# Kernel optimization log

Measured on AMD Instinct MI355X. Metric: run time of the kernel, lower is better.

## Reference

```python
import jax, jax.numpy as jnp
import numpy as np

NUM_HEADS = 16
NEG_INF = -9e15


def setup_inputs() -> dict:
    key = jax.random.key(0)
    k1, k2, k3 = jax.random.split(key, 3)
    B, S, D = 2, 2048, 1024
    # xavier-uniform-ish init scale for weights
    lim_qkv = float(np.sqrt(6.0 / (D + 3 * D)))
    lim_o = float(np.sqrt(6.0 / (D + D)))
    return {
        "x": jax.random.normal(k1, (B, S, D), dtype=jnp.float32),
        "w_qkv": jax.random.uniform(k2, (3 * D, D), minval=-lim_qkv, maxval=lim_qkv, dtype=jnp.float32),
        "b_qkv": jnp.zeros((3 * D,), dtype=jnp.float32),
        "w_o": jax.random.uniform(k3, (D, D), minval=-lim_o, maxval=lim_o, dtype=jnp.float32),
        "b_o": jnp.zeros((D,), dtype=jnp.float32),
    }


def reference(x, w_qkv, b_qkv, w_o, b_o):
    B, S, D = x.shape
    H = NUM_HEADS
    hd = D // H
    # qkv projection: [B,S,3D]
    qkv = x @ w_qkv.T + b_qkv
    # -> [B, H, S, 3*hd], then split
    qkv = qkv.reshape(B, S, H, 3 * hd).transpose(0, 2, 1, 3)
    q, k, v = jnp.split(qkv, 3, axis=-1)  # each [B,H,S,hd]
    scale = 1.0 / jnp.sqrt(jnp.asarray(hd, dtype=x.dtype))
    logits = jnp.einsum("bhqd,bhkd->bhqk", q, k) * scale
    attn = jax.nn.softmax(logits, axis=-1)
    vals = jnp.einsum("bhqk,bhkd->bhqd", attn, v)
    vals = vals.transpose(0, 2, 1, 3).reshape(B, S, D)
    return vals @ w_o.T + b_o
```

## Files before the change

kernel.cpp:

```cpp
#include <hip/hip_runtime.h>
#include <math.h>

#define NHEADS 16
#define HD 64

typedef __attribute__((ext_vector_type(8))) _Float16 half8;
typedef __attribute__((ext_vector_type(4))) _Float16 half4;
typedef __attribute__((ext_vector_type(4))) float f32x4;
typedef __attribute__((ext_vector_type(16))) float f32x16;
typedef __attribute__((ext_vector_type(4))) unsigned int u32x4;

__device__ inline void load_lds16(const void* g, void* l) {
    __builtin_amdgcn_global_load_lds(
        (const __attribute__((address_space(1))) unsigned int*)g,
        (__attribute__((address_space(3))) unsigned int*)l, 16, 0, 0);
}
__device__ inline void pl32swap(unsigned int& x, unsigned int& y) {
    asm volatile("v_permlane32_swap_b32 %0, %1" : "+v"(x), "+v"(y));
}

#define NX  4194304
#define NWQ 3145728
#define NWO 1048576
__global__ void cvt_all(const float* __restrict__ x, const float* __restrict__ wq,
                        const float* __restrict__ wo, _Float16* __restrict__ xf,
                        _Float16* __restrict__ wqf, _Float16* __restrict__ wof) {
    int i = (blockIdx.x * blockDim.x + threadIdx.x) * 8;
    const float* src; _Float16* dst; int off;
    if (i < NX)            { src = x;  dst = xf;  off = i; }
    else if (i < NX + NWQ) { src = wq; dst = wqf; off = i - NX; }
    else                   { src = wo; dst = wof; off = i - (NX + NWQ); }
    float4 a = *(const float4*)(src + off);
    float4 b = *(const float4*)(src + off + 4);
    half8 h;
    h[0] = (_Float16)a.x; h[1] = (_Float16)a.y; h[2] = (_Float16)a.z; h[3] = (_Float16)a.w;
    h[4] = (_Float16)b.x; h[5] = (_Float16)b.y; h[6] = (_Float16)b.z; h[7] = (_Float16)b.w;
    *(half8*)(dst + off) = h;
}

#define GEMM_SETUP(K, NTILE)                                                           \
    const int tid = threadIdx.x;                                                       \
    const int l = tid & 63, w = tid >> 6;                                              \
    const int wr = w >> 1, wc = w & 1;                                                 \
    const int nwg = gridDim.x * gridDim.y;                                             \
    const int bid = blockIdx.y * gridDim.x + blockIdx.x;                               \
    const int swz = (bid & 7) * (nwg >> 3) + (bid >> 3);                               \
    const int m0 = (swz / gridDim.x) * 128, n0 = (swz % gridDim.x) * (NTILE);          \
    const int srow = tid >> 2;                                                         \
    const int schunk = (tid & 3) ^ ((srow >> 1) & 3);                                  \
    const size_t gA0 = (size_t)(m0 + srow) * K + schunk * 8;                           \
    const size_t gA1 = gA0 + (size_t)64 * K;                                           \
    const size_t gB0 = (size_t)(n0 + srow) * K + schunk * 8;                           \
    unsigned char* ldsW = smem + w * 1024;                                             \
    const int col16 = l & 15, kc = l >> 4;                                             \
    const int ra0 = wr * 64 + col16;                                                   \
    const int offA = ra0 * 64 + ((kc ^ ((ra0 >> 1) & 3)) * 16);

#define QSCALE 0.18033688f
__global__ __launch_bounds__(256, 2) void gemm_qkv(
    const _Float16* __restrict__ A, const _Float16* __restrict__ B,
    const float* __restrict__ bias,
    _Float16* __restrict__ Qf, _Float16* __restrict__ Kf,
    _Float16* __restrict__ VfT, int K) {
    __shared__ __align__(1024) unsigned char smem[49152];
    GEMM_SETUP(K, 128)
    const size_t gB1 = gB0 + (size_t)64 * K;
    const int rb0 = wc * 64 + col16;
    const int offB = rb0 * 64 + ((kc ^ ((rb0 >> 1) & 3)) * 16);
    f32x4 acc[4][4] = {};

#define GSTAGE(k0_, buf_)                                                              \
    load_lds16(A + gA0 + (k0_), ldsW + (buf_) * 16384 + 0);                            \
    load_lds16(A + gA1 + (k0_), ldsW + (buf_) * 16384 + 4096);                         \
    load_lds16(B + gB0 + (k0_), ldsW + (buf_) * 16384 + 8192);                         \
    load_lds16(B + gB1 + (k0_), ldsW + (buf_) * 16384 + 12288);
#define GSTEP(s_, buf_, VM, dostage)                                                   \
    asm volatile("s_waitcnt " VM ::: "memory");                                        \
    __builtin_amdgcn_sched_barrier(0);                                                 \
    __builtin_amdgcn_s_barrier();                                                      \
    if (dostage) { GSTAGE(((s_) + 2) * 32, ((buf_) + 2) % 3) }                         \
    {                                                                                  \
        const unsigned char* bs = smem + (buf_) * 16384;                               \
        half8 af[4], bf[4];                                                            \
        _Pragma("unroll")                                                              \
        for (int m = 0; m < 4; ++m) af[m] = *(const half8*)(bs + offA + m * 1024);     \
        _Pragma("unroll")                                                              \
        for (int n = 0; n < 4; ++n) bf[n] = *(const half8*)(bs + 8192 + offB + n * 1024); \
        _Pragma("unroll")                                                              \
        for (int m = 0; m < 4; ++m)                                                    \
            _Pragma("unroll")                                                          \
            for (int n = 0; n < 4; ++n)                                                \
                acc[m][n] = __builtin_amdgcn_mfma_f32_16x16x32_f16(af[m], bf[n], acc[m][n], 0, 0, 0); \
    }

    GSTAGE(0, 0)
    GSTAGE(32, 1)
    for (int t = 0; t < 30; t += 3) {
        GSTEP(t, 0, "vmcnt(4)", 1)
        GSTEP(t + 1, 1, "vmcnt(4)", 1)
        GSTEP(t + 2, 2, "vmcnt(4)", 1)
    }
    GSTEP(30, 0, "vmcnt(4)", 0)
    GSTEP(31, 1, "vmcnt(0)", 0)
#undef GSTAGE
#undef GSTEP

    const int rowb = m0 + wr * 64 + (l >> 4) * 4;
    const int colb = n0 + wc * 64 + col16;
    #pragma unroll
    for (int n = 0; n < 4; ++n) {
        int col = colb + n * 16;
        int h = col / 192;
        int rem = col - h * 192;
        int part = rem >> 6, d = rem & 63;
        float bv = bias[col];
        #pragma unroll
        for (int m = 0; m < 4; ++m) {
            int r0 = rowb + m * 16;
            int b = r0 >> 11, s0r = r0 & 2047;
            int bh = b * 16 + h;
            if (part == 0) {
                #pragma unroll
                for (int j = 0; j < 4; ++j)
                    Qf[((size_t)bh * 2048 + s0r + j) * 64 + d] =
                        (_Float16)((acc[m][n][j] + bv) * QSCALE);
            } else if (part == 1) {
                #pragma unroll
                for (int j = 0; j < 4; ++j)
                    Kf[((size_t)bh * 2048 + s0r + j) * 64 + d] = (_Float16)(acc[m][n][j] + bv);
            } else {
                half4 pk;
                pk[0] = (_Float16)(acc[m][n][0] + bv);
                pk[1] = (_Float16)(acc[m][n][1] + bv);
                pk[2] = (_Float16)(acc[m][n][2] + bv);
                pk[3] = (_Float16)(acc[m][n][3] + bv);
                *(half4*)&VfT[((size_t)bh * 64 + d) * 2048 + s0r] = pk;
            }
        }
    }
}

__global__ __launch_bounds__(256, 2) void gemm_o(
    const _Float16* __restrict__ A, const _Float16* __restrict__ B,
    const float* __restrict__ bias, float* __restrict__ C,
    int M, int N, int K) {
    __shared__ __align__(1024) unsigned char smem[36864];
    GEMM_SETUP(K, 64)
    const int rb0 = wc * 32 + col16;
    const int offB = rb0 * 64 + ((kc ^ ((rb0 >> 1) & 3)) * 16);
    f32x4 acc[4][2] = {};

#define OSTAGE(k0_, buf_)                                                              \
    load_lds16(A + gA0 + (k0_), ldsW + (buf_) * 12288 + 0);                            \
    load_lds16(A + gA1 + (k0_), ldsW + (buf_) * 12288 + 4096);                         \
    load_lds16(B + gB0 + (k0_), ldsW + (buf_) * 12288 + 8192);
#define OSTEP(s_, buf_, VM, dostage)                                                   \
    asm volatile("s_waitcnt " VM ::: "memory");                                        \
    __builtin_amdgcn_sched_barrier(0);                                                 \
    __builtin_amdgcn_s_barrier();                                                      \
    if (dostage) { OSTAGE(((s_) + 2) * 32, ((buf_) + 2) % 3) }                         \
    {                                                                                  \
        const unsigned char* bs = smem + (buf_) * 12288;                               \
        half8 af[4], bf[2];                                                            \
        _Pragma("unroll")                                                              \
        for (int m = 0; m < 4; ++m) af[m] = *(const half8*)(bs + offA + m * 1024);     \
        _Pragma("unroll")                                                              \
        for (int n = 0; n < 2; ++n) bf[n] = *(const half8*)(bs + 8192 + offB + n * 1024); \
        _Pragma("unroll")                                                              \
        for (int m = 0; m < 4; ++m)                                                    \
            _Pragma("unroll")                                                          \
            for (int n = 0; n < 2; ++n)                                                \
                acc[m][n] = __builtin_amdgcn_mfma_f32_16x16x32_f16(af[m], bf[n], acc[m][n], 0, 0, 0); \
    }

    OSTAGE(0, 0)
    OSTAGE(32, 1)
    for (int t = 0; t < 30; t += 3) {
        OSTEP(t, 0, "vmcnt(3)", 1)
        OSTEP(t + 1, 1, "vmcnt(3)", 1)
        OSTEP(t + 2, 2, "vmcnt(3)", 1)
    }
    OSTEP(30, 0, "vmcnt(3)", 0)
    OSTEP(31, 1, "vmcnt(0)", 0)
#undef OSTAGE
#undef OSTEP

    const int rowb = m0 + wr * 64 + (l >> 4) * 4;
    const int colb = n0 + wc * 32 + col16;
    float bv[2];
    #pragma unroll
    for (int n = 0; n < 2; ++n) bv[n] = bias[colb + n * 16];
    #pragma unroll
    for (int m = 0; m < 4; ++m)
        #pragma unroll
        for (int j = 0; j < 4; ++j) {
            float* crow = C + (size_t)(rowb + m * 16 + j) * N + colb;
            #pragma unroll
            for (int n = 0; n < 2; ++n) crow[n * 16] = acc[m][n][j] + bv[n];
        }
}

__global__ __launch_bounds__(512, 2) void mfma_attn(
    const _Float16* __restrict__ Qf, const _Float16* __restrict__ Kf,
    const _Float16* __restrict__ VfT, _Float16* __restrict__ vals) {
    __shared__ __align__(1024) unsigned char smem[49152];
    const int tid = threadIdx.x;
    const int l = tid & 63, w = tid >> 6;
    const int l31 = l & 31, hl = l >> 5;
    const int hwbid = blockIdx.y * gridDim.x + blockIdx.x;
    const int q_t = (hwbid >> 3) & 7;
    const int bh = (hwbid & 7) + ((hwbid >> 6) << 3);
    const int q0 = q_t * 256;
    const int h = bh & 15, b = bh >> 4;

    half8 qf[4];
    {
        const _Float16* qp = Qf + ((size_t)bh * 2048 + q0 + w * 32 + l31) * 64 + hl * 8;
        #pragma unroll
        for (int c = 0; c < 4; ++c) qf[c] = *(const half8*)(qp + c * 16);
    }
    f32x16 zvec = {};
    f32x16 o0 = {}, o1 = {};
    float mshift = 0.f, lsum = 0.f;

    const _Float16* Kg = Kf + (size_t)bh * 2048 * 64;
    const _Float16* Vg = VfT + (size_t)bh * 64 * 2048;

    int offK, offV;
    {
        int row2 = w * 4 + (l >> 4);
        int slot = (l & 15) ^ (row2 & 15);
        int row = row2 * 2 + (slot >> 3);
        int chunk = slot & 7;
        offK = row * 64 + chunk * 8;
        offV = row * 2048 + chunk * 8;
    }
    const int sbase = (l31 & 1) * 8;
    const int xr = (l31 >> 1) & 15;
    const int rb0 = (l31 >> 1) * 256;

    #define STAGE(kt0, buf)                                                            \
        {                                                                              \
            unsigned char* bK = smem + (buf) * 8192 + w * 1024;                        \
            unsigned char* bV = smem + 24576 + (buf) * 8192 + w * 1024;                \
            load_lds16(Kg + (size_t)(kt0) * 64 + offK, bK);                            \
            load_lds16(Vg + (kt0) + offV, bV);                                         \
        }

    #define QK_TILE(kb, D0, D1)                                                        \
        {                                                                              \
            const unsigned char* Ksb_ = smem + (kb) * 8192;                            \
            {                                                                          \
                int chOff = ((sbase + hl) ^ xr) << 4;                                  \
                half8 k0_ = *(const half8*)(Ksb_ + rb0 + chOff);                       \
                half8 k1_ = *(const half8*)(Ksb_ + rb0 + 4096 + chOff);                \
                D0 = __builtin_amdgcn_mfma_f32_32x32x16_f16(k0_, qf[0], zvec, 0, 0, 0);\
                D1 = __builtin_amdgcn_mfma_f32_32x32x16_f16(k1_, qf[0], zvec, 0, 0, 0);\
            }                                                                          \
            _Pragma("unroll")                                                          \
            for (int kc = 1; kc < 4; ++kc) {                                           \
                int chOff = ((sbase + kc * 2 + hl) ^ xr) << 4;                         \
                half8 k0_ = *(const half8*)(Ksb_ + rb0 + chOff);                       \
                half8 k1_ = *(const half8*)(Ksb_ + rb0 + 4096 + chOff);                \
                D0 = __builtin_amdgcn_mfma_f32_32x32x16_f16(k0_, qf[kc], D0, 0, 0, 0); \
                D1 = __builtin_amdgcn_mfma_f32_32x32x16_f16(k1_, qf[kc], D1, 0, 0, 0); \
            }                                                                          \
        }

    #define SMPV(S0, S1, vb_)                                                          \
        {                                                                              \
            const unsigned char* Vsb_ = smem + 24576 + (vb_) * 8192;                   \
            if (__any(mshift != 0.f)) {                                                \
                _Pragma("unroll")                                                      \
                for (int r = 0; r < 16; ++r) { S0[r] -= mshift; S1[r] -= mshift; }     \
            }                                                                          \
            float r0 = 0.f, r1 = 0.f, r2 = 0.f, r3 = 0.f;                              \
            unsigned int a[2][8];                                                      \
            _Pragma("unroll")                                                          \
            for (int j = 0; j < 8; ++j) {                                              \
                float p0 = __builtin_amdgcn_exp2f(S0[2 * j]);                          \
                float p1 = __builtin_amdgcn_exp2f(S0[2 * j + 1]);                      \
                float q0_ = __builtin_amdgcn_exp2f(S1[2 * j]);                         \
                float q1_ = __builtin_amdgcn_exp2f(S1[2 * j + 1]);                     \
                r0 += p0; r1 += p1; r2 += q0_; r3 += q1_;                              \
                a[0][j] = __builtin_bit_cast(unsigned int, __builtin_amdgcn_cvt_pkrtz(p0, p1));   \
                a[1][j] = __builtin_bit_cast(unsigned int, __builtin_amdgcn_cvt_pkrtz(q0_, q1_)); \
            }                                                                          \
            float rsum = (r0 + r1) + (r2 + r3);                                        \
            if (__any(rsum > 32768.f)) {                                               \
                float pmax = S0[0];                                                    \
                _Pragma("unroll")                                                      \
                for (int r = 1; r < 16; ++r) pmax = fmaxf(pmax, S0[r]);                \
                _Pragma("unroll")                                                      \
                for (int r = 0; r < 16; ++r) pmax = fmaxf(pmax, S1[r]);                \
                pmax = fmaxf(pmax, __shfl_xor(pmax, 32, 64));                          \
                float d_ = fmaxf(pmax, 0.f);                                           \
                float corr = __builtin_amdgcn_exp2f(-d_);                              \
                _Pragma("unroll")                                                      \
                for (int r = 0; r < 16; ++r) { S0[r] -= d_; S1[r] -= d_; }             \
                _Pragma("unroll")                                                      \
                for (int r = 0; r < 16; ++r) { o0[r] *= corr; o1[r] *= corr; }         \
                lsum *= corr;                                                          \
                mshift += d_;                                                          \
                r0 = r1 = r2 = r3 = 0.f;                                               \
                _Pragma("unroll")                                                      \
                for (int j = 0; j < 8; ++j) {                                          \
                    float p0 = __builtin_amdgcn_exp2f(S0[2 * j]);                      \
                    float p1 = __builtin_amdgcn_exp2f(S0[2 * j + 1]);                  \
                    float q0_ = __builtin_amdgcn_exp2f(S1[2 * j]);                     \
                    float q1_ = __builtin_amdgcn_exp2f(S1[2 * j + 1]);                 \
                    r0 += p0; r1 += p1; r2 += q0_; r3 += q1_;                          \
                    a[0][j] = __builtin_bit_cast(unsigned int, __builtin_amdgcn_cvt_pkrtz(p0, p1));   \
                    a[1][j] = __builtin_bit_cast(unsigned int, __builtin_amdgcn_cvt_pkrtz(q0_, q1_)); \
                }                                                                      \
                rsum = (r0 + r1) + (r2 + r3);                                          \
            }                                                                          \
            lsum += rsum;                                                              \
            _Pragma("unroll")                                                          \
            for (int c = 0; c < 2; ++c) {                                              \
                pl32swap(a[c][0], a[c][2]);                                            \
                pl32swap(a[c][1], a[c][3]);                                            \
                pl32swap(a[c][4], a[c][6]);                                            \
                pl32swap(a[c][5], a[c][7]);                                            \
            }                                                                          \
            _Pragma("unroll")                                                          \
            for (int kk = 0; kk < 4; ++kk) {                                           \
                u32x4 pw;                                                              \
                pw.x = a[kk >> 1][(kk & 1) * 4 + 0];                                   \
                pw.y = a[kk >> 1][(kk & 1) * 4 + 1];                                   \
                pw.z = a[kk >> 1][(kk & 1) * 4 + 2];                                   \
                pw.w = a[kk >> 1][(kk & 1) * 4 + 3];                                   \
                half8 pf = __builtin_bit_cast(half8, pw);                              \
                int chOff = ((sbase + kk * 2 + hl) ^ xr) << 4;                         \
                half8 v0 = *(const half8*)(Vsb_ + rb0 + chOff);                        \
                half8 v1 = *(const half8*)(Vsb_ + rb0 + 4096 + chOff);                 \
                o0 = __builtin_amdgcn_mfma_f32_32x32x16_f16(v0, pf, o0, 0, 0, 0);      \
                o1 = __builtin_amdgcn_mfma_f32_32x32x16_f16(v1, pf, o1, 0, 0, 0);      \
            }                                                                          \
        }

    #define AITER(tt, kb, VM, dostage)                                                 \
        asm volatile("s_waitcnt " VM ::: "memory");                                    \
        __builtin_amdgcn_sched_barrier(0);                                             \
        __builtin_amdgcn_s_barrier();                                                  \
        if (dostage) STAGE(((tt) + 2) * 64, ((kb) + 2) % 3)                            \
        QK_TILE(kb, sS0, sS1)                                                          \
        SMPV(sS0, sS1, kb)

    STAGE(0, 0)
    STAGE(64, 1)
    f32x16 sS0, sS1;
    for (int t = 0; t < 30; t += 3) {
        AITER(t, 0, "vmcnt(2)", 1)
        AITER(t + 1, 1, "vmcnt(2)", 1)
        AITER(t + 2, 2, "vmcnt(2)", 1)
    }
    AITER(30, 0, "vmcnt(2)", 0)
    AITER(31, 1, "vmcnt(0)", 0)

    lsum += __shfl_xor(lsum, 32, 64);
    float inv = 1.f / lsum;
    size_t orow = ((size_t)(b * 2048 + q0 + w * 32 + l31)) * 1024 + h * 64;
    #pragma unroll
    for (int dc = 0; dc < 2; ++dc) {
        const f32x16* op = dc ? &o1 : &o0;
        #pragma unroll
        for (int rq = 0; rq < 4; ++rq) {
            int d0 = dc * 32 + rq * 8 + hl * 4;
            half4 hv;
            #pragma unroll
            for (int j = 0; j < 4; ++j) hv[j] = (_Float16)((*op)[rq * 4 + j] * inv);
            *(half4*)(vals + orow + d0) = hv;
        }
    }
}

extern "C" void kernel_launch(void* const* d_in, const int* in_sizes, int n_in,
                              void* d_out, int out_size, void* d_ws, size_t ws_size,
                              hipStream_t stream) {
    const float* x     = (const float*)d_in[0];
    const float* w_qkv = (const float*)d_in[1];
    const float* b_qkv = (const float*)d_in[2];
    const float* w_o   = (const float*)d_in[3];
    const float* b_o   = (const float*)d_in[4];
    float* out = (float*)d_out;

    const int B = 2, S = 2048, D = 1024;
    const int M = B * S;
    const int N1 = 3 * D;
    const int BH = B * NHEADS;

    _Float16* xf  = (_Float16*)d_ws;
    _Float16* wqf = xf  + (size_t)M * D;
    _Float16* wof = wqf + (size_t)N1 * D;
    _Float16* Qf  = wof + (size_t)D * D;
    _Float16* Kf  = Qf  + (size_t)BH * S * HD;
    _Float16* VfT = Kf  + (size_t)BH * S * HD;
    _Float16* vals = xf;

    cvt_all<<<(NX + NWQ + NWO) / 2048, 256, 0, stream>>>(x, w_qkv, w_o, xf, wqf, wof);

    gemm_qkv<<<dim3(N1 / 128, M / 128), 256, 0, stream>>>(xf, wqf, b_qkv, Qf, Kf, VfT, D);

    mfma_attn<<<dim3(S / 256, BH), 512, 0, stream>>>(Qf, Kf, VfT, vals);

    gemm_o<<<dim3(D / 64, M / 128), 256, 0, stream>>>(vals, wof, b_o, out, M, D, D);
}
```

Measured before the change: 107.2 us.

## Rewrite QKV GEMM with 256x256 tiles, 8 waves and phased double-buffered loads

Replaces the 128x128 QKV projection GEMM (256 threads, triple-buffered K=32 stages) with a 256x256 tile per workgroup. It uses 8 waves and a double-buffered K=64 pipeline whose global-to-LDS loads are split into four compute phases, with s_setprio raised around the MFMA blocks. The larger tile is meant to raise arithmetic intensity and cut redundant global/LDS traffic per output. In exchange it uses 128KB of LDS, so only one block fits per CU, and the grid shrinks to 192 workgroups, which leaves some CUs idle. It also renames a loop variable in the attention kernel and inlines the old setup macro into gemm_o.

```diff
diff --git a/kernel.cpp b/kernel.cpp
--- a/kernel.cpp
+++ b/kernel.cpp
@@ -38,74 +38,107 @@
     *(half8*)(dst + off) = h;
 }
 
-#define GEMM_SETUP(K, NTILE)                                                           \
-    const int tid = threadIdx.x;                                                       \
-    const int l = tid & 63, w = tid >> 6;                                              \
-    const int wr = w >> 1, wc = w & 1;                                                 \
-    const int nwg = gridDim.x * gridDim.y;                                             \
-    const int bid = blockIdx.y * gridDim.x + blockIdx.x;                               \
-    const int swz = (bid & 7) * (nwg >> 3) + (bid >> 3);                               \
-    const int m0 = (swz / gridDim.x) * 128, n0 = (swz % gridDim.x) * (NTILE);          \
-    const int srow = tid >> 2;                                                         \
-    const int schunk = (tid & 3) ^ ((srow >> 1) & 3);                                  \
-    const size_t gA0 = (size_t)(m0 + srow) * K + schunk * 8;                           \
-    const size_t gA1 = gA0 + (size_t)64 * K;                                           \
-    const size_t gB0 = (size_t)(n0 + srow) * K + schunk * 8;                           \
-    unsigned char* ldsW = smem + w * 1024;                                             \
-    const int col16 = l & 15, kc = l >> 4;                                             \
-    const int ra0 = wr * 64 + col16;                                                   \
-    const int offA = ra0 * 64 + ((kc ^ ((ra0 >> 1) & 3)) * 16);
-
 #define QSCALE 0.18033688f
-__global__ __launch_bounds__(256, 2) void gemm_qkv(
+__global__ __launch_bounds__(512, 2) void gemm_qkv(
     const _Float16* __restrict__ A, const _Float16* __restrict__ B,
     const float* __restrict__ bias,
     _Float16* __restrict__ Qf, _Float16* __restrict__ Kf,
-    _Float16* __restrict__ VfT, int K) {
-    __shared__ __align__(1024) unsigned char smem[49152];
-    GEMM_SETUP(K, 128)
-    const size_t gB1 = gB0 + (size_t)64 * K;
-    const int rb0 = wc * 64 + col16;
-    const int offB = rb0 * 64 + ((kc ^ ((rb0 >> 1) & 3)) * 16);
-    f32x4 acc[4][4] = {};
-
-#define GSTAGE(k0_, buf_)                                                              \
-    load_lds16(A + gA0 + (k0_), ldsW + (buf_) * 16384 + 0);                            \
-    load_lds16(A + gA1 + (k0_), ldsW + (buf_) * 16384 + 4096);                         \
-    load_lds16(B + gB0 + (k0_), ldsW + (buf_) * 16384 + 8192);                         \
-    load_lds16(B + gB1 + (k0_), ldsW + (buf_) * 16384 + 12288);
-#define GSTEP(s_, buf_, VM, dostage)                                                   \
-    asm volatile("s_waitcnt " VM ::: "memory");                                        \
-    __builtin_amdgcn_sched_barrier(0);                                                 \
-    __builtin_amdgcn_s_barrier();                                                      \
-    if (dostage) { GSTAGE(((s_) + 2) * 32, ((buf_) + 2) % 3) }                         \
-    {                                                                                  \
-        const unsigned char* bs = smem + (buf_) * 16384;                               \
-        half8 af[4], bf[4];                                                            \
-        _Pragma("unroll")                                                              \
-        for (int m = 0; m < 4; ++m) af[m] = *(const half8*)(bs + offA + m * 1024);     \
-        _Pragma("unroll")                                                              \
-        for (int n = 0; n < 4; ++n) bf[n] = *(const half8*)(bs + 8192 + offB + n * 1024); \
-        _Pragma("unroll")                                                              \
-        for (int m = 0; m < 4; ++m)                                                    \
-            _Pragma("unroll")                                                          \
-            for (int n = 0; n < 4; ++n)                                                \
-                acc[m][n] = __builtin_amdgcn_mfma_f32_16x16x32_f16(af[m], bf[n], acc[m][n], 0, 0, 0); \
-    }
-
-    GSTAGE(0, 0)
-    GSTAGE(32, 1)
-    for (int t = 0; t < 30; t += 3) {
-        GSTEP(t, 0, "vmcnt(4)", 1)
-        GSTEP(t + 1, 1, "vmcnt(4)", 1)
-        GSTEP(t + 2, 2, "vmcnt(4)", 1)
-    }
-    GSTEP(30, 0, "vmcnt(4)", 0)
-    GSTEP(31, 1, "vmcnt(0)", 0)
-#undef GSTAGE
-#undef GSTEP
-
-    const int rowb = m0 + wr * 64 + (l >> 4) * 4;
+    _Float16* __restrict__ VfT) {
+    __shared__ __align__(1024) unsigned char smem[131072];
+    const int tid = threadIdx.x;
+    const int l = tid & 63, w = tid >> 6;
+    const int wr = w >> 2, wc = w & 3;
+    const int col16 = l & 15, kc = l >> 4;
+    const int bid = blockIdx.y * gridDim.x + blockIdx.x;
+    const int swz = (bid & 7) * 24 + (bid >> 3);
+    const int m0 = (swz / 12) * 256, n0 = (swz % 12) * 256;
+
+    const int srcRow = w * 8 + (l >> 3);
+    const int srcChunk = ((l & 7) ^ (l >> 3)) * 8;
+    size_t aSrc[4], bSrc[4];
+    #pragma unroll
+    for (int q = 0; q < 4; ++q) {
+        aSrc[q] = (size_t)(m0 + q * 64 + srcRow) * 1024 + srcChunk;
+        bSrc[q] = (size_t)(n0 + q * 64 + srcRow) * 1024 + srcChunk;
+    }
+    const int ldsLane = w * 1024;
+
+    const int swzl = col16 & 7;
+    const int chOff0 = ((kc) ^ swzl) << 4;
+    const int chOff1 = ((4 + kc) ^ swzl) << 4;
+    int rowA[8], rowB[4];
+    #pragma unroll
+    for (int f = 0; f < 8; ++f) rowA[f] = (wr * 128 + f * 16 + col16) * 128;
+    #pragma unroll
+    for (int g = 0; g < 4; ++g) rowB[g] = 65536 + (wc * 64 + g * 16 + col16) * 128;
+
+    f32x4 acc[8][4] = {};
+
+#define SU_A(q_, tt_) load_lds16(A + aSrc[q_] + (tt_) * 64, \
+        smem + ((tt_) & 1) * 32768 + (q_) * 8192 + ldsLane);
+#define SU_B(q_, tt_) load_lds16(B + bSrc[q_] + (tt_) * 64, \
+        smem + 65536 + ((tt_) & 1) * 32768 + (q_) * 8192 + ldsLane);
+
+#define VMW2 asm volatile("s_waitcnt vmcnt(2)" ::: "memory");
+#define VMW4 asm volatile("s_waitcnt vmcnt(4)" ::: "memory");
+#define VMW0 asm volatile("s_waitcnt vmcnt(0)" ::: "memory");
+
+#define PH(mh_, nh_, bufOff_, VMWSTMT, STAGES) { \
+    VMWSTMT \
+    __builtin_amdgcn_sched_barrier(0); \
+    __builtin_amdgcn_s_barrier(); \
+    __builtin_amdgcn_sched_barrier(0); \
+    half8 af[4][2], bf[2][2]; \
+    _Pragma("unroll") \
+    for (int f = 0; f < 4; ++f) { \
+        const unsigned char* ap = smem + (bufOff_) + rowA[(mh_) * 4 + f]; \
+        af[f][0] = *(const half8*)(ap + chOff0); \
+        af[f][1] = *(const half8*)(ap + chOff1); \
+    } \
+    _Pragma("unroll") \
+    for (int g = 0; g < 2; ++g) { \
+        const unsigned char* bp = smem + (bufOff_) + rowB[(nh_) * 2 + g]; \
+        bf[g][0] = *(const half8*)(bp + chOff0); \
+        bf[g][1] = *(const half8*)(bp + chOff1); \
+    } \
+    STAGES \
+    asm volatile("s_waitcnt lgkmcnt(0)" ::: "memory"); \
+    __builtin_amdgcn_sched_barrier(0); \
+    __builtin_amdgcn_s_setprio(1); \
+    _Pragma("unroll") \
+    for (int f = 0; f < 4; ++f) \
+        _Pragma("unroll") \
+        for (int g = 0; g < 2; ++g) { \
+            acc[(mh_) * 4 + f][(nh_) * 2 + g] = __builtin_amdgcn_mfma_f32_16x16x32_f16( \
+                af[f][0], bf[g][0], acc[(mh_) * 4 + f][(nh_) * 2 + g], 0, 0, 0); \
+            acc[(mh_) * 4 + f][(nh_) * 2 + g] = __builtin_amdgcn_mfma_f32_16x16x32_f16( \
+                af[f][1], bf[g][1], acc[(mh_) * 4 + f][(nh_) * 2 + g], 0, 0, 0); \
+        } \
+    __builtin_amdgcn_s_setprio(0); }
+
+    SU_B(0, 0) SU_B(1, 0) SU_B(2, 0) SU_B(3, 0)
+    SU_A(0, 0) SU_A(2, 0) SU_A(1, 0) SU_A(3, 0)
+
+    for (int t = 0; t < 15; ++t) {
+        const int bufOff = (t & 1) * 32768;
+        PH(0, 0, bufOff, VMW2, { SU_B(0, t + 1) SU_B(1, t + 1) })
+        PH(0, 1, bufOff, ,     { SU_B(2, t + 1) SU_B(3, t + 1) })
+        PH(1, 0, bufOff, VMW4, { SU_A(0, t + 1) SU_A(2, t + 1) })
+        PH(1, 1, bufOff, ,     { SU_A(1, t + 1) SU_A(3, t + 1) })
+    }
+    PH(0, 0, 32768, VMW2, {})
+    PH(0, 1, 32768, ,     {})
+    PH(1, 0, 32768, VMW0, {})
+    PH(1, 1, 32768, ,     {})
+
+#undef SU_A
+#undef SU_B
+#undef VMW2
+#undef VMW4
+#undef VMW0
+#undef PH
+
+    const int rowb = m0 + wr * 128 + (l >> 4) * 4;
     const int colb = n0 + wc * 64 + col16;
     #pragma unroll
     for (int n = 0; n < 4; ++n) {
@@ -115,7 +148,7 @@
         int part = rem >> 6, d = rem & 63;
         float bv = bias[col];
         #pragma unroll
-        for (int m = 0; m < 4; ++m) {
+        for (int m = 0; m < 8; ++m) {
             int r0 = rowb + m * 16;
             int b = r0 >> 11, s0r = r0 & 2047;
             int bh = b * 16 + h;
@@ -145,7 +178,22 @@
     const float* __restrict__ bias, float* __restrict__ C,
     int M, int N, int K) {
     __shared__ __align__(1024) unsigned char smem[36864];
-    GEMM_SETUP(K, 64)
+    const int tid = threadIdx.x;
+    const int l = tid & 63, w = tid >> 6;
+    const int wr = w >> 1, wc = w & 1;
+    const int nwg = gridDim.x * gridDim.y;
+    const int bid = blockIdx.y * gridDim.x + blockIdx.x;
+    const int swz = (bid & 7) * (nwg >> 3) + (bid >> 3);
+    const int m0 = (swz / gridDim.x) * 128, n0 = (swz % gridDim.x) * 64;
+    const int srow = tid >> 2;
+    const int schunk = (tid & 3) ^ ((srow >> 1) & 3);
+    const size_t gA0 = (size_t)(m0 + srow) * K + schunk * 8;
+    const size_t gA1 = gA0 + (size_t)64 * K;
+    const size_t gB0 = (size_t)(n0 + srow) * K + schunk * 8;
+    unsigned char* ldsW = smem + w * 1024;
+    const int col16 = l & 15, kc = l >> 4;
+    const int ra0 = wr * 64 + col16;
+    const int offA = ra0 * 64 + ((kc ^ ((ra0 >> 1) & 3)) * 16);
     const int rb0 = wc * 32 + col16;
     const int offB = rb0 * 64 + ((kc ^ ((rb0 >> 1) & 3)) * 16);
     f32x4 acc[4][2] = {};
@@ -258,12 +306,12 @@
                 D1 = __builtin_amdgcn_mfma_f32_32x32x16_f16(k1_, qf[0], zvec, 0, 0, 0);\
             }                                                                          \
             _Pragma("unroll")                                                          \
-            for (int kc = 1; kc < 4; ++kc) {                                           \
-                int chOff = ((sbase + kc * 2 + hl) ^ xr) << 4;                         \
+            for (int kcq = 1; kcq < 4; ++kcq) {                                        \
+                int chOff = ((sbase + kcq * 2 + hl) ^ xr) << 4;                        \
                 half8 k0_ = *(const half8*)(Ksb_ + rb0 + chOff);                       \
                 half8 k1_ = *(const half8*)(Ksb_ + rb0 + 4096 + chOff);                \
-                D0 = __builtin_amdgcn_mfma_f32_32x32x16_f16(k0_, qf[kc], D0, 0, 0, 0); \
-                D1 = __builtin_amdgcn_mfma_f32_32x32x16_f16(k1_, qf[kc], D1, 0, 0, 0); \
+                D0 = __builtin_amdgcn_mfma_f32_32x32x16_f16(k0_, qf[kcq], D0, 0, 0, 0);\
+                D1 = __builtin_amdgcn_mfma_f32_32x32x16_f16(k1_, qf[kcq], D1, 0, 0, 0);\
             }                                                                          \
         }
 
@@ -400,7 +448,7 @@
 
     cvt_all<<<(NX + NWQ + NWO) / 2048, 256, 0, stream>>>(x, w_qkv, w_o, xf, wqf, wof);
 
-    gemm_qkv<<<dim3(N1 / 128, M / 128), 256, 0, stream>>>(xf, wqf, b_qkv, Qf, Kf, VfT, D);
+    gemm_qkv<<<dim3(12, 16), 512, 0, stream>>>(xf, wqf, b_qkv, Qf, Kf, VfT);
 
     mfma_attn<<<dim3(S / 256, BH), 512, 0, stream>>>(Qf, Kf, VfT, vals);
 
```

Result: faster. 104.8 us (-2.3%).
